# Kernel optimization log

Hardware: AMD Instinct MI355X
Metric: run time of the kernel (lower is better)

Reference implementation:

```python
import math
import jax, jax.numpy as jnp
import numpy as np

D = 128   # per-head dim == model dim
H = 16    # heads
B = 2
S = 2048


def setup_inputs() -> dict:
    key = jax.random.key(0)
    ks = jax.random.split(key, 6)
    sc = 0.02
    x = jax.random.normal(ks[0], (B, S, D), dtype=jnp.float32)
    mask = jax.random.randint(ks[1], (B, 1, S, S), 0, 2, dtype=jnp.int32)
    Wq = jax.random.normal(ks[2], (D * H, D), dtype=jnp.float32) * sc
    Wk = jax.random.normal(ks[3], (D * H, D), dtype=jnp.float32) * sc
    Wv = jax.random.normal(ks[4], (D * H, D), dtype=jnp.float32) * sc
    Wd = jax.random.normal(ks[5], (D, D * H), dtype=jnp.float32) * sc
    return {
        "x": x, "mask": mask,
        "Wq": Wq, "bq": jnp.zeros((D * H,), jnp.float32),
        "Wk": Wk, "bk": jnp.zeros((D * H,), jnp.float32),
        "Wv": Wv, "bv": jnp.zeros((D * H,), jnp.float32),
        "Wd": Wd, "bd": jnp.zeros((D,), jnp.float32),
    }


def _split_heads(t):
    # (B, S, H*D) -> (B, H, S, D)
    b, s, _ = t.shape
    return t.reshape(b, s, H, D).transpose(0, 2, 1, 3)


def reference(x, mask, Wq, bq, Wk, bk, Wv, bv, Wd, bd):
    # torch Linear: y = x @ W.T + b
    q = _split_heads(x @ Wq.T + bq)   # (B,H,S,D)
    k = _split_heads(x @ Wk.T + bk)
    v = _split_heads(x @ Wv.T + bv)
    scores = jnp.einsum("bhsd,bhtd->bhst", q, k) / math.sqrt(D)
    scores = scores + mask.astype(scores.dtype) * (-1e9)
    weights = jax.nn.softmax(scores, axis=-1)          # (B,H,S,S)
    ctx = jnp.einsum("bhst,bhtd->bhsd", weights, v)    # (B,H,S,D)
    concat = ctx.transpose(0, 2, 1, 3).reshape(x.shape[0], x.shape[1], H * D)
    out = concat @ Wd.T + bd                           # (B,S,D)
    return out, weights
```

## Files before the change

### kernel.cpp

```cpp
#include <hip/hip_runtime.h>
#include <hip/hip_bf16.h>


using short8 = __attribute__((ext_vector_type(8))) short;
using f32x4  = __attribute__((ext_vector_type(4))) float;

#define DEVFN static __device__ __forceinline__

DEVFN unsigned short f2bf(float f) {
    unsigned int u = __builtin_bit_cast(unsigned int, f);
    u += 0x7fffu + ((u >> 16) & 1u);
    return (unsigned short)(u >> 16);
}
DEVFN float bf2f(unsigned short b) {
    unsigned int u = ((unsigned int)b) << 16;
    return __builtin_bit_cast(float, u);
}

template<int ROWS>
DEVFN void stage_bf16(const unsigned short* __restrict__ g, long ld,
                      unsigned short* lds, int tid) {
#pragma unroll
    for (int j = 0; j < ROWS / 32; ++j) {
        int c = tid + j * 256;
        int r = c >> 3, kc = (c & 7) << 3;
        *reinterpret_cast<uint4*>(lds + r * 64 + kc) =
            *reinterpret_cast<const uint4*>(g + (long)r * ld + kc);
    }
}

template<int MF, int NF>
DEVFN void mfma_tile(const unsigned short* As, const unsigned short* Bs,
                     f32x4 (&acc)[MF][NF], int lane) {
    int lr = lane & 15, lg = lane >> 4;
#pragma unroll
    for (int kk = 0; kk < 2; ++kk) {
        short8 a[MF], b[NF];
#pragma unroll
        for (int m = 0; m < MF; ++m)
            a[m] = *reinterpret_cast<const short8*>(As + (m * 16 + lr) * 64 + kk * 32 + lg * 8);
#pragma unroll
        for (int n = 0; n < NF; ++n)
            b[n] = *reinterpret_cast<const short8*>(Bs + (n * 16 + lr) * 64 + kk * 32 + lg * 8);
#pragma unroll
        for (int m = 0; m < MF; ++m)
#pragma unroll
            for (int n = 0; n < NF; ++n)
                acc[m][n] = __builtin_amdgcn_mfma_f32_16x16x32_bf16(a[m], b[n], acc[m][n], 0, 0, 0);
    }
}

__global__ __launch_bounds__(256) void k_prep(
        const float* __restrict__ x, const float* __restrict__ wq,
        const float* __restrict__ wk, const float* __restrict__ wv,
        const float* __restrict__ wd,
        unsigned short* __restrict__ xb, unsigned short* __restrict__ wqb,
        unsigned short* __restrict__ wkb, unsigned short* __restrict__ wvb,
        unsigned short* __restrict__ wdb, float* __restrict__ rowsum) {
    int i = blockIdx.x * 256 + threadIdx.x;
    if (i < 524288)        xb[i] = f2bf(x[i]);
    else if (i < 786432)   wqb[i - 524288]  = f2bf(wq[i - 524288]);
    else if (i < 1048576)  wkb[i - 786432]  = f2bf(wk[i - 786432]);
    else if (i < 1310720)  wvb[i - 1048576] = f2bf(wv[i - 1048576]);
    else if (i < 1572864)  wdb[i - 1310720] = f2bf(wd[i - 1310720]);
    else if (i < 1638400)  rowsum[i - 1572864] = 0.0f;
}

__global__ __launch_bounds__(256) void k_qkv(
        const unsigned short* __restrict__ xb, const unsigned short* __restrict__ wqb,
        const unsigned short* __restrict__ wkb, const unsigned short* __restrict__ wvb,
        const float* __restrict__ bq, const float* __restrict__ bk,
        const float* __restrict__ bv,
        unsigned short* __restrict__ Qb, unsigned short* __restrict__ Kb,
        unsigned short* __restrict__ Vtb) {
    __shared__ __align__(16) char smem[32768];
    unsigned short* As = (unsigned short*)smem;
    unsigned short* Bs = (unsigned short*)(smem + 16384);
    unsigned short* Cs = (unsigned short*)smem;
    int tid = threadIdx.x, lane = tid & 63, wid = tid >> 6;
    int wr = wid >> 1, wc = wid & 1;
    int lr = lane & 15, lg = lane >> 4;
    int mt = blockIdx.x, nt = blockIdx.y, z = blockIdx.z;
    const unsigned short* Wb = (z == 0) ? wqb : ((z == 1) ? wkb : wvb);
    const float* bias = (z == 0) ? bq : ((z == 1) ? bk : bv);
    const unsigned short* gA = xb + (long)mt * 128 * 128;
    const unsigned short* gB = Wb + (long)nt * 128 * 128;
    f32x4 acc[4][4] = {};
#pragma unroll
    for (int kt = 0; kt < 2; ++kt) {
        __syncthreads();
        stage_bf16<128>(gA + kt * 64, 128, As, tid);
        stage_bf16<128>(gB + kt * 64, 128, Bs, tid);
        __syncthreads();
        mfma_tile<4, 4>(As + wr * 64 * 64, Bs + wc * 64 * 64, acc, lane);
    }
    __syncthreads();
#pragma unroll
    for (int n = 0; n < 4; ++n) {
        int col = wc * 64 + n * 16 + lr;
        float bval = bias[nt * 128 + col];
#pragma unroll
        for (int m = 0; m < 4; ++m)
#pragma unroll
            for (int r = 0; r < 4; ++r) {
                int row = wr * 64 + m * 16 + lg * 4 + r;
                Cs[row * 128 + col] = f2bf(acc[m][n][r] + bval);
            }
    }
    __syncthreads();
    int rg0 = mt * 128;
    int b = rg0 >> 11, s0 = rg0 & 2047, h = nt;
    if (z < 2) {
        unsigned short* dst = ((z == 0) ? Qb : Kb) + ((long)(b * 16 + h) * 2048 + s0) * 128;
#pragma unroll
        for (int j = 0; j < 8; ++j) {
            int c = tid + j * 256;
            int r = c >> 4, cc2 = (c & 15) << 3;
            *reinterpret_cast<uint4*>(dst + (long)r * 128 + cc2) =
                *reinterpret_cast<uint4*>(Cs + r * 128 + cc2);
        }
    } else {
        unsigned short* dst = Vtb + (long)(b * 16 + h) * 128 * 2048;
#pragma unroll
        for (int j = 0; j < 8; ++j) {
            int c = tid + j * 256;
            int d = c >> 4, sl = (c & 15) << 3;
            unsigned int w0 = (unsigned int)Cs[(sl + 0) * 128 + d] | ((unsigned int)Cs[(sl + 1) * 128 + d] << 16);
            unsigned int w1 = (unsigned int)Cs[(sl + 2) * 128 + d] | ((unsigned int)Cs[(sl + 3) * 128 + d] << 16);
            unsigned int w2 = (unsigned int)Cs[(sl + 4) * 128 + d] | ((unsigned int)Cs[(sl + 5) * 128 + d] << 16);
            unsigned int w3 = (unsigned int)Cs[(sl + 6) * 128 + d] | ((unsigned int)Cs[(sl + 7) * 128 + d] << 16);
            *reinterpret_cast<uint4*>(dst + (long)d * 2048 + s0 + sl) = make_uint4(w0, w1, w2, w3);
        }
    }
}

__global__ __launch_bounds__(256) void k_scores(
        const unsigned short* __restrict__ Qb, const unsigned short* __restrict__ Kb,
        const int* __restrict__ mask, float* __restrict__ wout,
        float* __restrict__ rowsum) {
    __shared__ __align__(16) char smem[32768];
    unsigned short* As = (unsigned short*)smem;
    unsigned short* Bs = (unsigned short*)(smem + 16384);
    unsigned short* Cs = (unsigned short*)smem;
    int tid = threadIdx.x, lane = tid & 63, wid = tid >> 6;
    int wr = wid >> 1, wc = wid & 1;
    int lr = lane & 15, lg = lane >> 4;
    int z = blockIdx.z, b = z >> 4;
    int s0 = blockIdx.x * 128, t0 = blockIdx.y * 128;
    const unsigned short* gA = Qb + (long)z * 2048 * 128 + (long)s0 * 128;
    const unsigned short* gB = Kb + (long)z * 2048 * 128 + (long)t0 * 128;
    f32x4 acc[4][4] = {};
#pragma unroll
    for (int kt = 0; kt < 2; ++kt) {
        __syncthreads();
        stage_bf16<128>(gA + kt * 64, 128, As, tid);
        stage_bf16<128>(gB + kt * 64, 128, Bs, tid);
        __syncthreads();
        mfma_tile<4, 4>(As + wr * 64 * 64, Bs + wc * 64 * 64, acc, lane);
    }
    __syncthreads();
    const float SCALE = 0.08838834764831845f;
    const int* gM = mask + (long)b * 2048 * 2048;
#pragma unroll
    for (int m = 0; m < 4; ++m)
#pragma unroll
        for (int n = 0; n < 4; ++n)
#pragma unroll
            for (int r = 0; r < 4; ++r) {
                int row = wr * 64 + m * 16 + lg * 4 + r;
                int col = wc * 64 + n * 16 + lr;
                int mk = gM[(long)(s0 + row) * 2048 + t0 + col];
                acc[m][n][r] = mk ? 0.0f : __expf(acc[m][n][r] * SCALE);
            }
    float* rsz = rowsum + z * 2048 + s0;
#pragma unroll
    for (int m = 0; m < 4; ++m)
#pragma unroll
        for (int r = 0; r < 4; ++r) {
            float sv = acc[m][0][r] + acc[m][1][r] + acc[m][2][r] + acc[m][3][r];
            sv += __shfl_xor(sv, 1);
            sv += __shfl_xor(sv, 2);
            sv += __shfl_xor(sv, 4);
            sv += __shfl_xor(sv, 8);
            if (lr == 0) {
                int row = wr * 64 + m * 16 + lg * 4 + r;
                atomicAdd(rsz + row, sv);
            }
        }
#pragma unroll
    for (int m = 0; m < 4; ++m)
#pragma unroll
        for (int n = 0; n < 4; ++n)
#pragma unroll
            for (int r = 0; r < 4; ++r) {
                int row = wr * 64 + m * 16 + lg * 4 + r;
                int col = wc * 64 + n * 16 + lr;
                Cs[row * 128 + col] = f2bf(acc[m][n][r]);
            }
    __syncthreads();
    float* dst = wout + (long)z * 2048 * 2048 + (long)s0 * 2048 + t0;
#pragma unroll
    for (int j = 0; j < 8; ++j) {
        int c = tid + j * 256;
        int r = c >> 4, cc2 = (c & 15) << 3;
        uint4 uv = *reinterpret_cast<uint4*>(Cs + r * 128 + cc2);
        float4 lo, hi;
        lo.x = bf2f((unsigned short)(uv.x & 0xffff)); lo.y = bf2f((unsigned short)(uv.x >> 16));
        lo.z = bf2f((unsigned short)(uv.y & 0xffff)); lo.w = bf2f((unsigned short)(uv.y >> 16));
        hi.x = bf2f((unsigned short)(uv.z & 0xffff)); hi.y = bf2f((unsigned short)(uv.z >> 16));
        hi.z = bf2f((unsigned short)(uv.w & 0xffff)); hi.w = bf2f((unsigned short)(uv.w >> 16));
        *reinterpret_cast<float4*>(dst + (long)r * 2048 + cc2) = lo;
        *reinterpret_cast<float4*>(dst + (long)r * 2048 + cc2 + 4) = hi;
    }
}

__global__ __launch_bounds__(256) void k_ctx(
        float* __restrict__ wio, const float* __restrict__ rowsum,
        const unsigned short* __restrict__ Vtb, unsigned short* __restrict__ ccb) {
    __shared__ __align__(16) char smem[32768];
    unsigned short* As = (unsigned short*)smem;
    unsigned short* Bs = (unsigned short*)(smem + 16384);
    unsigned short* Cs = (unsigned short*)smem;
    int tid = threadIdx.x, lane = tid & 63, wid = tid >> 6;
    int wr = wid >> 1, wc = wid & 1;
    int lr = lane & 15, lg = lane >> 4;
    int z = blockIdx.z, b = z >> 4, h = z & 15;
    int s0 = blockIdx.x * 128;
    float* gW = wio + (long)z * 2048 * 2048 + (long)s0 * 2048;
    const unsigned short* gV = Vtb + (long)z * 128 * 2048;
    const float* rs = rowsum + z * 2048 + s0;
    f32x4 acc[4][4] = {};
    for (int kt = 0; kt < 32; ++kt) {
        __syncthreads();
#pragma unroll
        for (int j = 0; j < 8; ++j) {
            int c = tid + j * 256;
            int r = c >> 4, kc = (c & 15) << 2;
            long off = (long)r * 2048 + kt * 64 + kc;
            float4 w = *reinterpret_cast<float4*>(gW + off);
            float inv = 1.0f / rs[r];
            w.x *= inv; w.y *= inv; w.z *= inv; w.w *= inv;
            *reinterpret_cast<float4*>(gW + off) = w;
            unsigned int p0 = (unsigned int)f2bf(w.x) | ((unsigned int)f2bf(w.y) << 16);
            unsigned int p1 = (unsigned int)f2bf(w.z) | ((unsigned int)f2bf(w.w) << 16);
            *reinterpret_cast<uint2*>(As + r * 64 + kc) = make_uint2(p0, p1);
        }
        stage_bf16<128>(gV + kt * 64, 2048, Bs, tid);
        __syncthreads();
        mfma_tile<4, 4>(As + wr * 64 * 64, Bs + wc * 64 * 64, acc, lane);
    }
    __syncthreads();
#pragma unroll
    for (int m = 0; m < 4; ++m)
#pragma unroll
        for (int n = 0; n < 4; ++n)
#pragma unroll
            for (int r = 0; r < 4; ++r) {
                int row = wr * 64 + m * 16 + lg * 4 + r;
                int col = wc * 64 + n * 16 + lr;
                Cs[row * 128 + col] = f2bf(acc[m][n][r]);
            }
    __syncthreads();
    unsigned short* dst = ccb + ((long)b * 2048 + s0) * 2048 + h * 128;
#pragma unroll
    for (int j = 0; j < 8; ++j) {
        int c = tid + j * 256;
        int r = c >> 4, cc2 = (c & 15) << 3;
        *reinterpret_cast<uint4*>(dst + (long)r * 2048 + cc2) =
            *reinterpret_cast<uint4*>(Cs + r * 128 + cc2);
    }
}

__global__ __launch_bounds__(256) void k_out(
        const unsigned short* __restrict__ ccb, const unsigned short* __restrict__ wdb,
        const float* __restrict__ bd, float* __restrict__ out) {
    __shared__ __align__(16) char smem[24576];
    unsigned short* As = (unsigned short*)smem;
    unsigned short* Bs = (unsigned short*)(smem + 8192);
    unsigned short* Cs = (unsigned short*)smem;
    int tid = threadIdx.x, lane = tid & 63, wid = tid >> 6;
    int wr = wid >> 1, wc = wid & 1;
    int lr = lane & 15, lg = lane >> 4;
    int mt = blockIdx.x;
    const unsigned short* gA = ccb + (long)mt * 64 * 2048;
    f32x4 acc[2][4] = {};
    for (int kt = 0; kt < 32; ++kt) {
        __syncthreads();
        stage_bf16<64>(gA + kt * 64, 2048, As, tid);
        stage_bf16<128>(wdb + kt * 64, 2048, Bs, tid);
        __syncthreads();
        mfma_tile<2, 4>(As + wr * 32 * 64, Bs + wc * 64 * 64, acc, lane);
    }
    __syncthreads();
#pragma unroll
    for (int n = 0; n < 4; ++n) {
        int col = wc * 64 + n * 16 + lr;
        float bval = bd[col];
#pragma unroll
        for (int m = 0; m < 2; ++m)
#pragma unroll
            for (int r = 0; r < 4; ++r) {
                int row = wr * 32 + m * 16 + lg * 4 + r;
                Cs[row * 128 + col] = f2bf(acc[m][n][r] + bval);
            }
    }
    __syncthreads();
    float* dst = out + (long)mt * 64 * 128;
#pragma unroll
    for (int j = 0; j < 8; ++j) {
        int c = tid + j * 256;
        int r = c >> 5, cc2 = (c & 31) << 2;
        uint2 uv = *reinterpret_cast<uint2*>(Cs + r * 128 + cc2);
        float4 o;
        o.x = bf2f((unsigned short)(uv.x & 0xffff));
        o.y = bf2f((unsigned short)(uv.x >> 16));
        o.z = bf2f((unsigned short)(uv.y & 0xffff));
        o.w = bf2f((unsigned short)(uv.y >> 16));
        *reinterpret_cast<float4*>(dst + r * 128 + cc2) = o;
    }
}

extern "C" void kernel_launch(void* const* d_in, const int* in_sizes, int n_in,
                              void* d_out, int out_size, void* d_ws, size_t ws_size,
                              hipStream_t stream) {
    const float* x  = (const float*)d_in[0];
    const int* mask = (const int*)d_in[1];
    const float* Wq = (const float*)d_in[2];
    const float* bq = (const float*)d_in[3];
    const float* Wk = (const float*)d_in[4];
    const float* bk = (const float*)d_in[5];
    const float* Wv = (const float*)d_in[6];
    const float* bv = (const float*)d_in[7];
    const float* Wd = (const float*)d_in[8];
    const float* bd = (const float*)d_in[9];

    float* out  = (float*)d_out;
    float* wout = out + 524288;

    char* ws = (char*)d_ws;
    unsigned short* xb   = (unsigned short*)(ws + 0);
    unsigned short* wqb  = (unsigned short*)(ws + 1048576);
    unsigned short* wkb  = (unsigned short*)(ws + 1572864);
    unsigned short* wvb  = (unsigned short*)(ws + 2097152);
    unsigned short* wdb  = (unsigned short*)(ws + 2621440);
    unsigned short* Qb   = (unsigned short*)(ws + 3145728);
    unsigned short* Kb   = (unsigned short*)(ws + 19922944);
    unsigned short* Vtb  = (unsigned short*)(ws + 36700160);
    unsigned short* ccb  = (unsigned short*)(ws + 53477376);
    float*          rsum = (float*)(ws + 70254592);

    k_prep<<<6400, 256, 0, stream>>>(x, Wq, Wk, Wv, Wd, xb, wqb, wkb, wvb, wdb, rsum);
    k_qkv<<<dim3(32, 16, 3), 256, 0, stream>>>(xb, wqb, wkb, wvb, bq, bk, bv, Qb, Kb, Vtb);
    k_scores<<<dim3(16, 16, 32), 256, 0, stream>>>(Qb, Kb, mask, wout, rsum);
    k_ctx<<<dim3(16, 1, 32), 256, 0, stream>>>(wout, rsum, Vtb, ccb);
    k_out<<<dim3(64, 1, 1), 256, 0, stream>>>(ccb, wdb, bd, out);
}
```

Measured before the change: 1.091 ms.

## Fuse scores, softmax and context into one two-pass attention kernel with bit-packed mask

Replaces the separate scores and context kernels with a single attention kernel. A first pass over K tiles computes the row sums of exp(scores); a second pass recomputes the scores, normalises them, writes the fp32 weights once and multiplies by V in the same loop. This removes the extra read and rewrite of the huge weights tensor and the atomic row-sum accumulation. The 1/sqrt(D) scale is folded into Q, and the int32 mask is packed into 64-bit ballot words by a new kernel to cut mask traffic. Other changes: the prep kernel is vectorised and now zeroes the output, and the output projection uses split-K with atomic adds. The cost is computing QK^T twice and relying on float atomics for the final output.

```diff
diff --git a/kernel.cpp b/kernel.cpp
--- a/kernel.cpp
+++ b/kernel.cpp
@@ -6,6 +6,9 @@
 using f32x4  = __attribute__((ext_vector_type(4))) float;
 
 #define DEVFN static __device__ __forceinline__
+
+#define SWZ256(row, colb) ((((row)) << 8) + ((colb) ^ ((((row)) & 7) << 4)))
+#define SWZ128(row, colb) ((((row)) << 7) + ((colb) ^ ((((row)) & 7) << 4)))
 
 DEVFN unsigned short f2bf(float f) {
     unsigned int u = __builtin_bit_cast(unsigned int, f);
@@ -53,17 +56,39 @@
 __global__ __launch_bounds__(256) void k_prep(
         const float* __restrict__ x, const float* __restrict__ wq,
         const float* __restrict__ wk, const float* __restrict__ wv,
-        const float* __restrict__ wd,
+        const float* __restrict__ wd, float* __restrict__ out,
         unsigned short* __restrict__ xb, unsigned short* __restrict__ wqb,
         unsigned short* __restrict__ wkb, unsigned short* __restrict__ wvb,
-        unsigned short* __restrict__ wdb, float* __restrict__ rowsum) {
-    int i = blockIdx.x * 256 + threadIdx.x;
-    if (i < 524288)        xb[i] = f2bf(x[i]);
-    else if (i < 786432)   wqb[i - 524288]  = f2bf(wq[i - 524288]);
-    else if (i < 1048576)  wkb[i - 786432]  = f2bf(wk[i - 786432]);
-    else if (i < 1310720)  wvb[i - 1048576] = f2bf(wv[i - 1048576]);
-    else if (i < 1572864)  wdb[i - 1310720] = f2bf(wd[i - 1310720]);
-    else if (i < 1638400)  rowsum[i - 1572864] = 0.0f;
+        unsigned short* __restrict__ wdb) {
+    int u = blockIdx.x * 256 + threadIdx.x;
+    const float* src; unsigned short* dst; int off;
+    if (u < 131072)       { src = x;  dst = xb;  off = u; }
+    else if (u < 196608)  { src = wq; dst = wqb; off = u - 131072; }
+    else if (u < 262144)  { src = wk; dst = wkb; off = u - 196608; }
+    else if (u < 327680)  { src = wv; dst = wvb; off = u - 262144; }
+    else if (u < 393216)  { src = wd; dst = wdb; off = u - 327680; }
+    else {
+        float4 z = make_float4(0.f, 0.f, 0.f, 0.f);
+        *reinterpret_cast<float4*>(out + (long)(u - 393216) * 4) = z;
+        return;
+    }
+    float4 v = *reinterpret_cast<const float4*>(src + (long)off * 4);
+    uint2 p;
+    p.x = (unsigned int)f2bf(v.x) | ((unsigned int)f2bf(v.y) << 16);
+    p.y = (unsigned int)f2bf(v.z) | ((unsigned int)f2bf(v.w) << 16);
+    *reinterpret_cast<uint2*>(dst + (long)off * 4) = p;
+}
+
+__global__ __launch_bounds__(256) void k_mask(
+        const int* __restrict__ mask, unsigned long long* __restrict__ bits) {
+    int wave = (blockIdx.x * 256 + threadIdx.x) >> 6;
+    int lane = threadIdx.x & 63;
+#pragma unroll
+    for (int i = 0; i < 16; ++i) {
+        long w = (long)wave * 16 + i;
+        unsigned long long bm = __ballot(mask[w * 64 + lane] != 0);
+        if (lane == 0) bits[w] = bm;
+    }
 }
 
 __global__ __launch_bounds__(256) void k_qkv(
@@ -85,6 +110,7 @@
     const float* bias = (z == 0) ? bq : ((z == 1) ? bk : bv);
     const unsigned short* gA = xb + (long)mt * 128 * 128;
     const unsigned short* gB = Wb + (long)nt * 128 * 128;
+    float scl = (z == 0) ? 0.08838834764831845f : 1.0f;
     f32x4 acc[4][4] = {};
 #pragma unroll
     for (int kt = 0; kt < 2; ++kt) {
@@ -104,7 +130,7 @@
 #pragma unroll
             for (int r = 0; r < 4; ++r) {
                 int row = wr * 64 + m * 16 + lg * 4 + r;
-                Cs[row * 128 + col] = f2bf(acc[m][n][r] + bval);
+                Cs[row * 128 + col] = f2bf((acc[m][n][r] + bval) * scl);
             }
     }
     __syncthreads();
@@ -134,140 +160,210 @@
     }
 }
 
-__global__ __launch_bounds__(256) void k_scores(
+__global__ __launch_bounds__(256, 2) void k_attn(
         const unsigned short* __restrict__ Qb, const unsigned short* __restrict__ Kb,
-        const int* __restrict__ mask, float* __restrict__ wout,
-        float* __restrict__ rowsum) {
-    __shared__ __align__(16) char smem[32768];
-    unsigned short* As = (unsigned short*)smem;
-    unsigned short* Bs = (unsigned short*)(smem + 16384);
-    unsigned short* Cs = (unsigned short*)smem;
+        const unsigned short* __restrict__ Vtb,
+        const unsigned long long* __restrict__ maskbits,
+        float* __restrict__ wout, unsigned short* __restrict__ ccb) {
+    __shared__ __align__(16) char smem[49152];
+    char* Ks = smem;
+    char* Vs = smem + 16384;
+    char* Ps = smem + 32768;
+    float* rs2 = (float*)(smem + 32768);
     int tid = threadIdx.x, lane = tid & 63, wid = tid >> 6;
     int wr = wid >> 1, wc = wid & 1;
     int lr = lane & 15, lg = lane >> 4;
-    int z = blockIdx.z, b = z >> 4;
-    int s0 = blockIdx.x * 128, t0 = blockIdx.y * 128;
-    const unsigned short* gA = Qb + (long)z * 2048 * 128 + (long)s0 * 128;
-    const unsigned short* gB = Kb + (long)z * 2048 * 128 + (long)t0 * 128;
-    f32x4 acc[4][4] = {};
-#pragma unroll
-    for (int kt = 0; kt < 2; ++kt) {
-        __syncthreads();
-        stage_bf16<128>(gA + kt * 64, 128, As, tid);
-        stage_bf16<128>(gB + kt * 64, 128, Bs, tid);
-        __syncthreads();
-        mfma_tile<4, 4>(As + wr * 64 * 64, Bs + wc * 64 * 64, acc, lane);
-    }
-    __syncthreads();
-    const float SCALE = 0.08838834764831845f;
-    const int* gM = mask + (long)b * 2048 * 2048;
+    int s0 = blockIdx.x * 128, z = blockIdx.y, b = z >> 4, h = z & 15;
+    const unsigned short* Qg = Qb + (long)z * 262144 + (long)s0 * 128;
+    const unsigned short* Kg = Kb + (long)z * 262144;
+    const unsigned short* Vg = Vtb + (long)z * 262144;
+    const unsigned long long* mb = maskbits + (long)b * 65536 + (long)s0 * 32;
+
+#pragma unroll
+    for (int j = 0; j < 8; ++j) {
+        int u = tid + j * 256;
+        int row = u >> 4, sl = u & 15;
+        *reinterpret_cast<uint4*>(smem + SWZ256(row, sl * 16)) =
+            *reinterpret_cast<const uint4*>(Qg + u * 8);
+    }
+    __syncthreads();
+    short8 aq[4][4];
 #pragma unroll
     for (int m = 0; m < 4; ++m)
 #pragma unroll
-        for (int n = 0; n < 4; ++n)
+        for (int kk = 0; kk < 4; ++kk)
+            aq[m][kk] = *reinterpret_cast<const short8*>(
+                smem + SWZ256(wr * 64 + m * 16 + lr, kk * 64 + lg * 16));
+    __syncthreads();
+
+    uint4 kreg[4], vreg[4];
+#pragma unroll
+    for (int j = 0; j < 4; ++j) {
+        int u = tid + j * 256;
+        kreg[j] = *reinterpret_cast<const uint4*>(Kg + u * 8);
+    }
+
+    float psum[4][4] = {};
+    for (int t = 0; t < 32; ++t) {
+#pragma unroll
+        for (int j = 0; j < 4; ++j) {
+            int u = tid + j * 256;
+            *reinterpret_cast<uint4*>(Ks + SWZ256(u >> 4, (u & 15) * 16)) = kreg[j];
+        }
+        if (t < 31) {
+#pragma unroll
+            for (int j = 0; j < 4; ++j) {
+                int u = tid + j * 256;
+                kreg[j] = *reinterpret_cast<const uint4*>(Kg + (t + 1) * 8192 + u * 8);
+            }
+        }
+        __syncthreads();
+        f32x4 sc[4][2] = {};
+#pragma unroll
+        for (int kk = 0; kk < 4; ++kk) {
+            short8 bk0 = *reinterpret_cast<const short8*>(Ks + SWZ256(wc * 32 + lr,      kk * 64 + lg * 16));
+            short8 bk1 = *reinterpret_cast<const short8*>(Ks + SWZ256(wc * 32 + 16 + lr, kk * 64 + lg * 16));
+#pragma unroll
+            for (int m = 0; m < 4; ++m) {
+                sc[m][0] = __builtin_amdgcn_mfma_f32_16x16x32_bf16(aq[m][kk], bk0, sc[m][0], 0, 0, 0);
+                sc[m][1] = __builtin_amdgcn_mfma_f32_16x16x32_bf16(aq[m][kk], bk1, sc[m][1], 0, 0, 0);
+            }
+        }
+#pragma unroll
+        for (int m = 0; m < 4; ++m)
+#pragma unroll
+            for (int r = 0; r < 4; ++r) {
+                unsigned long long w = mb[(wr * 64 + m * 16 + lg * 4 + r) * 32 + t];
+#pragma unroll
+                for (int n = 0; n < 2; ++n) {
+                    int bit = wc * 32 + n * 16 + lr;
+                    float e = ((w >> bit) & 1ull) ? 0.0f : __expf(sc[m][n][r]);
+                    psum[m][r] += e;
+                }
+            }
+        __syncthreads();
+    }
+
+#pragma unroll
+    for (int j = 0; j < 4; ++j) {
+        int u = tid + j * 256;
+        kreg[j] = *reinterpret_cast<const uint4*>(Kg + u * 8);
+        vreg[j] = *reinterpret_cast<const uint4*>(Vg + (long)(u >> 3) * 2048 + (u & 7) * 8);
+    }
+#pragma unroll
+    for (int m = 0; m < 4; ++m)
+#pragma unroll
+        for (int r = 0; r < 4; ++r) {
+            float v = psum[m][r];
+            v += __shfl_xor(v, 1); v += __shfl_xor(v, 2);
+            v += __shfl_xor(v, 4); v += __shfl_xor(v, 8);
+            if (lr == 0) rs2[wc * 128 + wr * 64 + m * 16 + lg * 4 + r] = v;
+        }
+    __syncthreads();
+    float inv[4][4];
+#pragma unroll
+    for (int m = 0; m < 4; ++m)
+#pragma unroll
+        for (int r = 0; r < 4; ++r) {
+            int row = wr * 64 + m * 16 + lg * 4 + r;
+            inv[m][r] = 1.0f / (rs2[row] + rs2[128 + row]);
+        }
+
+    f32x4 ctx[4][4] = {};
+    for (int t = 0; t < 32; ++t) {
+#pragma unroll
+        for (int j = 0; j < 4; ++j) {
+            int u = tid + j * 256;
+            *reinterpret_cast<uint4*>(Ks + SWZ256(u >> 4, (u & 15) * 16)) = kreg[j];
+            *reinterpret_cast<uint4*>(Vs + SWZ128(u >> 3, (u & 7) * 16)) = vreg[j];
+        }
+        if (t < 31) {
+#pragma unroll
+            for (int j = 0; j < 4; ++j) {
+                int u = tid + j * 256;
+                kreg[j] = *reinterpret_cast<const uint4*>(Kg + (t + 1) * 8192 + u * 8);
+                vreg[j] = *reinterpret_cast<const uint4*>(Vg + (long)(u >> 3) * 2048 + (t + 1) * 64 + (u & 7) * 8);
+            }
+        }
+        __syncthreads();
+        f32x4 sc[4][2] = {};
+#pragma unroll
+        for (int kk = 0; kk < 4; ++kk) {
+            short8 bk0 = *reinterpret_cast<const short8*>(Ks + SWZ256(wc * 32 + lr,      kk * 64 + lg * 16));
+            short8 bk1 = *reinterpret_cast<const short8*>(Ks + SWZ256(wc * 32 + 16 + lr, kk * 64 + lg * 16));
+#pragma unroll
+            for (int m = 0; m < 4; ++m) {
+                sc[m][0] = __builtin_amdgcn_mfma_f32_16x16x32_bf16(aq[m][kk], bk0, sc[m][0], 0, 0, 0);
+                sc[m][1] = __builtin_amdgcn_mfma_f32_16x16x32_bf16(aq[m][kk], bk1, sc[m][1], 0, 0, 0);
+            }
+        }
+#pragma unroll
+        for (int m = 0; m < 4; ++m)
 #pragma unroll
             for (int r = 0; r < 4; ++r) {
                 int row = wr * 64 + m * 16 + lg * 4 + r;
-                int col = wc * 64 + n * 16 + lr;
-                int mk = gM[(long)(s0 + row) * 2048 + t0 + col];
-                acc[m][n][r] = mk ? 0.0f : __expf(acc[m][n][r] * SCALE);
-            }
-    float* rsz = rowsum + z * 2048 + s0;
+                unsigned long long w = mb[row * 32 + t];
+#pragma unroll
+                for (int n = 0; n < 2; ++n) {
+                    int bit = wc * 32 + n * 16 + lr;
+                    float p = ((w >> bit) & 1ull) ? 0.0f : __expf(sc[m][n][r]);
+                    p *= inv[m][r];
+                    *reinterpret_cast<unsigned short*>(
+                        Ps + SWZ128(row, (wc * 32 + n * 16 + lr) * 2)) = f2bf(p);
+                }
+            }
+        __syncthreads();
+#pragma unroll
+        for (int kk = 0; kk < 2; ++kk) {
+            short8 ap[4], bv[4];
+#pragma unroll
+            for (int m = 0; m < 4; ++m)
+                ap[m] = *reinterpret_cast<const short8*>(Ps + SWZ128(wr * 64 + m * 16 + lr, kk * 64 + lg * 16));
+#pragma unroll
+            for (int n = 0; n < 4; ++n)
+                bv[n] = *reinterpret_cast<const short8*>(Vs + SWZ128(wc * 64 + n * 16 + lr, kk * 64 + lg * 16));
+#pragma unroll
+            for (int m = 0; m < 4; ++m)
+#pragma unroll
+                for (int n = 0; n < 4; ++n)
+                    ctx[m][n] = __builtin_amdgcn_mfma_f32_16x16x32_bf16(ap[m], bv[n], ctx[m][n], 0, 0, 0);
+        }
+        {
+            float* wg = wout + (long)z * 4194304 + (long)s0 * 2048 + t * 64;
+#pragma unroll
+            for (int j = 0; j < 4; ++j) {
+                int u = tid + j * 256;
+                int row = u >> 3, sl = u & 7;
+                uint4 pv = *reinterpret_cast<const uint4*>(Ps + SWZ128(row, sl * 16));
+                float4 lo, hi;
+                lo.x = bf2f((unsigned short)(pv.x & 0xffff)); lo.y = bf2f((unsigned short)(pv.x >> 16));
+                lo.z = bf2f((unsigned short)(pv.y & 0xffff)); lo.w = bf2f((unsigned short)(pv.y >> 16));
+                hi.x = bf2f((unsigned short)(pv.z & 0xffff)); hi.y = bf2f((unsigned short)(pv.z >> 16));
+                hi.z = bf2f((unsigned short)(pv.w & 0xffff)); hi.w = bf2f((unsigned short)(pv.w >> 16));
+                float* dst = wg + (long)row * 2048 + sl * 8;
+                *reinterpret_cast<float4*>(dst) = lo;
+                *reinterpret_cast<float4*>(dst + 4) = hi;
+            }
+        }
+        __syncthreads();
+    }
+
+    unsigned short* Cs = (unsigned short*)smem;
 #pragma unroll
     for (int m = 0; m < 4; ++m)
 #pragma unroll
-        for (int r = 0; r < 4; ++r) {
-            float sv = acc[m][0][r] + acc[m][1][r] + acc[m][2][r] + acc[m][3][r];
-            sv += __shfl_xor(sv, 1);
-            sv += __shfl_xor(sv, 2);
-            sv += __shfl_xor(sv, 4);
-            sv += __shfl_xor(sv, 8);
-            if (lr == 0) {
-                int row = wr * 64 + m * 16 + lg * 4 + r;
-                atomicAdd(rsz + row, sv);
-            }
-        }
-#pragma unroll
-    for (int m = 0; m < 4; ++m)
-#pragma unroll
         for (int n = 0; n < 4; ++n)
 #pragma unroll
-            for (int r = 0; r < 4; ++r) {
-                int row = wr * 64 + m * 16 + lg * 4 + r;
-                int col = wc * 64 + n * 16 + lr;
-                Cs[row * 128 + col] = f2bf(acc[m][n][r]);
-            }
-    __syncthreads();
-    float* dst = wout + (long)z * 2048 * 2048 + (long)s0 * 2048 + t0;
+            for (int r = 0; r < 4; ++r)
+                Cs[(wr * 64 + m * 16 + lg * 4 + r) * 128 + wc * 64 + n * 16 + lr] = f2bf(ctx[m][n][r]);
+    __syncthreads();
+    unsigned short* og = ccb + ((long)b * 2048 + s0) * 2048 + h * 128;
 #pragma unroll
     for (int j = 0; j < 8; ++j) {
-        int c = tid + j * 256;
-        int r = c >> 4, cc2 = (c & 15) << 3;
-        uint4 uv = *reinterpret_cast<uint4*>(Cs + r * 128 + cc2);
-        float4 lo, hi;
-        lo.x = bf2f((unsigned short)(uv.x & 0xffff)); lo.y = bf2f((unsigned short)(uv.x >> 16));
-        lo.z = bf2f((unsigned short)(uv.y & 0xffff)); lo.w = bf2f((unsigned short)(uv.y >> 16));
-        hi.x = bf2f((unsigned short)(uv.z & 0xffff)); hi.y = bf2f((unsigned short)(uv.z >> 16));
-        hi.z = bf2f((unsigned short)(uv.w & 0xffff)); hi.w = bf2f((unsigned short)(uv.w >> 16));
-        *reinterpret_cast<float4*>(dst + (long)r * 2048 + cc2) = lo;
-        *reinterpret_cast<float4*>(dst + (long)r * 2048 + cc2 + 4) = hi;
-    }
-}
-
-__global__ __launch_bounds__(256) void k_ctx(
-        float* __restrict__ wio, const float* __restrict__ rowsum,
-        const unsigned short* __restrict__ Vtb, unsigned short* __restrict__ ccb) {
-    __shared__ __align__(16) char smem[32768];
-    unsigned short* As = (unsigned short*)smem;
-    unsigned short* Bs = (unsigned short*)(smem + 16384);
-    unsigned short* Cs = (unsigned short*)smem;
-    int tid = threadIdx.x, lane = tid & 63, wid = tid >> 6;
-    int wr = wid >> 1, wc = wid & 1;
-    int lr = lane & 15, lg = lane >> 4;
-    int z = blockIdx.z, b = z >> 4, h = z & 15;
-    int s0 = blockIdx.x * 128;
-    float* gW = wio + (long)z * 2048 * 2048 + (long)s0 * 2048;
-    const unsigned short* gV = Vtb + (long)z * 128 * 2048;
-    const float* rs = rowsum + z * 2048 + s0;
-    f32x4 acc[4][4] = {};
-    for (int kt = 0; kt < 32; ++kt) {
-        __syncthreads();
-#pragma unroll
-        for (int j = 0; j < 8; ++j) {
-            int c = tid + j * 256;
-            int r = c >> 4, kc = (c & 15) << 2;
-            long off = (long)r * 2048 + kt * 64 + kc;
-            float4 w = *reinterpret_cast<float4*>(gW + off);
-            float inv = 1.0f / rs[r];
-            w.x *= inv; w.y *= inv; w.z *= inv; w.w *= inv;
-            *reinterpret_cast<float4*>(gW + off) = w;
-            unsigned int p0 = (unsigned int)f2bf(w.x) | ((unsigned int)f2bf(w.y) << 16);
-            unsigned int p1 = (unsigned int)f2bf(w.z) | ((unsigned int)f2bf(w.w) << 16);
-            *reinterpret_cast<uint2*>(As + r * 64 + kc) = make_uint2(p0, p1);
-        }
-        stage_bf16<128>(gV + kt * 64, 2048, Bs, tid);
-        __syncthreads();
-        mfma_tile<4, 4>(As + wr * 64 * 64, Bs + wc * 64 * 64, acc, lane);
-    }
-    __syncthreads();
-#pragma unroll
-    for (int m = 0; m < 4; ++m)
-#pragma unroll
-        for (int n = 0; n < 4; ++n)
-#pragma unroll
-            for (int r = 0; r < 4; ++r) {
-                int row = wr * 64 + m * 16 + lg * 4 + r;
-                int col = wc * 64 + n * 16 + lr;
-                Cs[row * 128 + col] = f2bf(acc[m][n][r]);
-            }
-    __syncthreads();
-    unsigned short* dst = ccb + ((long)b * 2048 + s0) * 2048 + h * 128;
-#pragma unroll
-    for (int j = 0; j < 8; ++j) {
-        int c = tid + j * 256;
-        int r = c >> 4, cc2 = (c & 15) << 3;
-        *reinterpret_cast<uint4*>(dst + (long)r * 2048 + cc2) =
-            *reinterpret_cast<uint4*>(Cs + r * 128 + cc2);
+        int u = tid + j * 256;
+        int row = u >> 4, sl = u & 15;
+        *reinterpret_cast<uint4*>(og + (long)row * 2048 + sl * 8) =
+            *reinterpret_cast<const uint4*>(Cs + row * 128 + sl * 8);
     }
 }
 
@@ -277,46 +373,31 @@
     __shared__ __align__(16) char smem[24576];
     unsigned short* As = (unsigned short*)smem;
     unsigned short* Bs = (unsigned short*)(smem + 8192);
-    unsigned short* Cs = (unsigned short*)smem;
     int tid = threadIdx.x, lane = tid & 63, wid = tid >> 6;
     int wr = wid >> 1, wc = wid & 1;
     int lr = lane & 15, lg = lane >> 4;
-    int mt = blockIdx.x;
-    const unsigned short* gA = ccb + (long)mt * 64 * 2048;
+    int mt = blockIdx.x, ks = blockIdx.y;
+    const unsigned short* gA = ccb + (long)mt * 64 * 2048 + ks * 512;
+    const unsigned short* gB = wdb + ks * 512;
     f32x4 acc[2][4] = {};
-    for (int kt = 0; kt < 32; ++kt) {
+    for (int kt = 0; kt < 8; ++kt) {
         __syncthreads();
         stage_bf16<64>(gA + kt * 64, 2048, As, tid);
-        stage_bf16<128>(wdb + kt * 64, 2048, Bs, tid);
+        stage_bf16<128>(gB + kt * 64, 2048, Bs, tid);
         __syncthreads();
         mfma_tile<2, 4>(As + wr * 32 * 64, Bs + wc * 64 * 64, acc, lane);
     }
-    __syncthreads();
 #pragma unroll
     for (int n = 0; n < 4; ++n) {
         int col = wc * 64 + n * 16 + lr;
-        float bval = bd[col];
+        float bval = (ks == 0) ? bd[col] : 0.0f;
 #pragma unroll
         for (int m = 0; m < 2; ++m)
 #pragma unroll
             for (int r = 0; r < 4; ++r) {
                 int row = wr * 32 + m * 16 + lg * 4 + r;
-                Cs[row * 128 + col] = f2bf(acc[m][n][r] + bval);
-            }
-    }
-    __syncthreads();
-    float* dst = out + (long)mt * 64 * 128;
-#pragma unroll
-    for (int j = 0; j < 8; ++j) {
-        int c = tid + j * 256;
-        int r = c >> 5, cc2 = (c & 31) << 2;
-        uint2 uv = *reinterpret_cast<uint2*>(Cs + r * 128 + cc2);
-        float4 o;
-        o.x = bf2f((unsigned short)(uv.x & 0xffff));
-        o.y = bf2f((unsigned short)(uv.x >> 16));
-        o.z = bf2f((unsigned short)(uv.y & 0xffff));
-        o.w = bf2f((unsigned short)(uv.y >> 16));
-        *reinterpret_cast<float4*>(dst + r * 128 + cc2) = o;
+                atomicAdd(out + (long)(mt * 64 + row) * 128 + col, acc[m][n][r] + bval);
+            }
     }
 }
 
@@ -347,11 +428,11 @@
     unsigned short* Kb   = (unsigned short*)(ws + 19922944);
     unsigned short* Vtb  = (unsigned short*)(ws + 36700160);
     unsigned short* ccb  = (unsigned short*)(ws + 53477376);
-    float*          rsum = (float*)(ws + 70254592);
-
-    k_prep<<<6400, 256, 0, stream>>>(x, Wq, Wk, Wv, Wd, xb, wqb, wkb, wvb, wdb, rsum);
+    unsigned long long* maskbits = (unsigned long long*)(ws + 0);
+
+    k_prep<<<2048, 256, 0, stream>>>(x, Wq, Wk, Wv, Wd, out, xb, wqb, wkb, wvb, wdb);
     k_qkv<<<dim3(32, 16, 3), 256, 0, stream>>>(xb, wqb, wkb, wvb, bq, bk, bv, Qb, Kb, Vtb);
-    k_scores<<<dim3(16, 16, 32), 256, 0, stream>>>(Qb, Kb, mask, wout, rsum);
-    k_ctx<<<dim3(16, 1, 32), 256, 0, stream>>>(wout, rsum, Vtb, ccb);
-    k_out<<<dim3(64, 1, 1), 256, 0, stream>>>(ccb, wdb, bd, out);
-}
+    k_mask<<<2048, 256, 0, stream>>>(mask, maskbits);
+    k_attn<<<dim3(16, 32), 256, 0, stream>>>(Qb, Kb, Vtb, maskbits, wout, ccb);
+    k_out<<<dim3(64, 4), 256, 0, stream>>>(ccb, wdb, bd, out);
+}
```

New measurement: 1.178 ms. 8.0% more time.
